# Kernel tuning notes

Hardware: AMD Instinct MI355X
Metric: run time of the kernel (lower is better)

Reference implementation:

```python
import jax, jax.numpy as jnp
import numpy as np

B, C, D, H, W = 4, 128, 24, 24, 24
P = 64


def _sparse_table(x):
    # Range-max sparse table along the last axis: level k holds max over
    # windows [i, i+2^k). Levels 0..3 (window sizes 1,2,4,8) suffice because
    # adaptive-pool region lengths are ceil(n/2) <= 12 for crop length n <= 24.
    tabs = [x]
    for k in range(1, 4):
        h = 1 << (k - 1)
        prev = tabs[-1]
        tabs.append(jnp.maximum(prev, jnp.roll(prev, -h, axis=-1)))
    return jnp.stack(tabs, 0)


def _klev(n):
    # floor(log2(n)) for n in [1, 12]
    return ((n >= 2).astype(jnp.int32) + (n >= 4).astype(jnp.int32)
            + (n >= 8).astype(jnp.int32))


def _bounds(s, e, size):
    # AdaptiveMaxPool (output size 2) region bounds along one axis.
    # crop is [s, min(e, size)); region o: [s + floor(o*n/2), s + ceil((o+1)*n/2))
    e = jnp.minimum(e, size)
    n = e - s  # crop length, always >= 2 here
    o = jnp.arange(2)
    start = s[..., None] + (o * n[..., None]) // 2
    end = s[..., None] + ((o + 1) * n[..., None] + 1) // 2
    return start, end


def _qmax(T, idx_prefix, sa, se):
    # Range max over [sa, se) along the last axis via two overlapping
    # power-of-two windows from the sparse table T ([L, ..., S]).
    k = _klev(se - sa)
    i2 = se - jnp.left_shift(1, k)
    lo = T[(k,) + idx_prefix + (Ellipsis, sa)]
    hi = T[(k,) + idx_prefix + (Ellipsis, i2)]
    return jnp.maximum(lo, hi)


def _crop_pool(fm, corners, scale):
    b, c, d, h, w = fm.shape
    p = corners.shape[1]
    # int(x/scale) with non-negative ints == floor division
    p1 = jnp.clip(corners[:, :, 0, :] // scale, 0, 21)   # [B,P,3]
    p2r = corners[:, :, 1, :] // scale
    p2 = jnp.where(p2r - p1 >= 2, p2r, p1 + 2)           # [B,P,3], p2 >= p1+2

    bi = jnp.arange(b)[:, None, None]                    # [B,1,1]
    pi = jnp.arange(p)[None, :, None]                    # [1,P,1]

    # reduce z (W axis): [B,C,D,H,W] -> [B,P,2(oz),C,D,H]
    sa, se = _bounds(p1[..., 2], p2[..., 2], w)
    r = _qmax(_sparse_table(fm), (bi,), sa, se)
    # reduce y (H axis): -> [B,P,2(oy),2(oz),C,D]
    sa, se = _bounds(p1[..., 1], p2[..., 1], h)
    r = _qmax(_sparse_table(r), (bi, pi), sa, se)
    # reduce x (D axis): -> [B,P,2(ox),2(oy),2(oz),C]
    sa, se = _bounds(p1[..., 0], p2[..., 0], d)
    r = _qmax(_sparse_table(r), (bi, pi), sa, se)
    # -> [B,P,C,2,2,2]
    return jnp.transpose(r, (0, 1, 5, 2, 3, 4))


def setup_inputs() -> dict:
    key = jax.random.key(0)
    k1, k2 = jax.random.split(key)
    fm = jax.random.normal(k1, (B, C, D, H, W), dtype=jnp.float32)
    corners = jax.random.randint(k2, (B, P, 2, 3), 0, 96, dtype=jnp.int32)
    return {"fm": fm, "corners": corners, "scale": 4}


def reference(fm, corners, scale):
    return _crop_pool(fm, corners, scale)
```

## Files before the change

### kernel.cpp

```cpp
#include <hip/hip_runtime.h>
#include <math.h>

#define Bc 4
#define Cc 128
#define Pc 64
#define PLANE 576
#define VOL   13824
#define NI    (-INFINITY)


struct Acc { float v00, v01, v10, v11; };

template<int RMODE>
__device__ __forceinline__ void upd(Acc& a, float t0, float t1) {
    if (RMODE != 1) { a.v00 = fmaxf(a.v00, t0); a.v01 = fmaxf(a.v01, t1); }
    if (RMODE != 0) { a.v10 = fmaxf(a.v10, t0); a.v11 = fmaxf(a.v11, t1); }
}

template<int RMODE>
__device__ __forceinline__ void plane_chunk(
    const float* __restrict__ p0, const float* __restrict__ p1,
    const float* __restrict__ p2, const float* __restrict__ p3,
    int fcl, const float4& B0, const float4& B1,
    Acc& a0, Acc& a1, Acc& a2, Acc& a3)
{
    float4 v0 = *(const float4*)(p0 + fcl);
    float4 v1 = *(const float4*)(p1 + fcl);
    float4 v2 = *(const float4*)(p2 + fcl);
    float4 v3 = *(const float4*)(p3 + fcl);
#define TREE(v, B) fmaxf(fmaxf((v).x + (B).x, (v).y + (B).y),              \
                         fmaxf((v).z + (B).z, (v).w + (B).w))
    upd<RMODE>(a0, TREE(v0, B0), TREE(v0, B1));
    upd<RMODE>(a1, TREE(v1, B0), TREE(v1, B1));
    upd<RMODE>(a2, TREE(v2, B0), TREE(v2, B1));
    upd<RMODE>(a3, TREE(v3, B0), TREE(v3, B1));
#undef TREE
}

__device__ __forceinline__ float oct_reduce(const float o[8], int lane) {
    const bool b0 = lane & 1, b1 = lane & 2, b2 = lane & 4;
    float m0 = fmaxf(b0 ? o[1] : o[0], __shfl_xor(b0 ? o[0] : o[1], 1));
    float m1 = fmaxf(b0 ? o[3] : o[2], __shfl_xor(b0 ? o[2] : o[3], 1));
    float m2 = fmaxf(b0 ? o[5] : o[4], __shfl_xor(b0 ? o[4] : o[5], 1));
    float m3 = fmaxf(b0 ? o[7] : o[6], __shfl_xor(b0 ? o[6] : o[7], 1));
    float n0 = fmaxf(b1 ? m1 : m0, __shfl_xor(b1 ? m0 : m1, 2));
    float n1 = fmaxf(b1 ? m3 : m2, __shfl_xor(b1 ? m2 : m3, 2));
    float v  = fmaxf(b2 ? n1 : n0, __shfl_xor(b2 ? n0 : n1, 4));
    v = fmaxf(v, __shfl_xor(v, 8));
    v = fmaxf(v, __shfl_xor(v, 16));
    v = fmaxf(v, __shfl_xor(v, 32));
    return v;
}

__global__ __launch_bounds__(256) void crop_pool_kernel(
    const float* __restrict__ fm, const int* __restrict__ corners,
    const int* __restrict__ scale_p, float* __restrict__ out)
{
    const int lane = threadIdx.x & 63;
    const int wid  = threadIdx.x >> 6;
    const int bp   = blockIdx.x >> 3;
    const int cg   = blockIdx.x & 7;
    const int slot = cg * 4 + wid;
    const int b    = bp >> 6;

    const float inv = 1.0f / (float)scale_p[0];

    int s[3], e[3], m0a[3], m1a[3];
#pragma unroll
    for (int k = 0; k < 3; ++k) {
        int c0 = corners[(bp * 2 + 0) * 3 + k];
        int c1 = corners[(bp * 2 + 1) * 3 + k];
        int p1v = (int)((float)c0 * inv);
        p1v = p1v > 21 ? 21 : p1v;
        int p2v = (int)((float)c1 * inv);
        if (p2v - p1v < 2) p2v = p1v + 2;
        int ee = p2v < 24 ? p2v : 24;
        int n  = ee - p1v;
        s[k]   = __builtin_amdgcn_readfirstlane(p1v);
        e[k]   = __builtin_amdgcn_readfirstlane(ee);
        m0a[k] = __builtin_amdgcn_readfirstlane(p1v + ((n + 1) >> 1));
        m1a[k] = __builtin_amdgcn_readfirstlane(p1v + (n >> 1));
    }

    const int sh  = s[1], eh = e[1], nh = eh - sh;
    const int m0h = m0a[1], m1h = m1a[1];
    const int sw  = s[2], ew = e[2], m0w = m0a[2], m1w = m1a[2];

    const int qb = sw & ~3;
    const int Q  = ((sw & 3) + (ew - sw) + 3) >> 2;
    const int R  = 64 / Q;

    const unsigned M = (65536u + (unsigned)Q - 1) / (unsigned)Q;
    const int r = (int)(((unsigned)lane * M) >> 16);
    const int q = lane - r * Q;
    const int wbase = qb + 4 * q;

    const bool c1p = nh > R;
    const bool c2p = nh > 2 * R;

    float4 B0, B1;
    {
        int wt;
        wt = wbase + 0;
        B0.x = (wt >= sw  && wt < m0w) ? 0.0f : NI;
        B1.x = (wt >= m1w && wt < ew ) ? 0.0f : NI;
        wt = wbase + 1;
        B0.y = (wt >= sw  && wt < m0w) ? 0.0f : NI;
        B1.y = (wt >= m1w && wt < ew ) ? 0.0f : NI;
        wt = wbase + 2;
        B0.z = (wt >= sw  && wt < m0w) ? 0.0f : NI;
        B1.z = (wt >= m1w && wt < ew ) ? 0.0f : NI;
        wt = wbase + 3;
        B0.w = (wt >= sw  && wt < m0w) ? 0.0f : NI;
        B1.w = (wt >= m1w && wt < ew ) ? 0.0f : NI;
    }

    int  fcl[3];
    bool h0m[3], h1m[3];
#pragma unroll
    for (int K = 0; K < 3; ++K) {
        const int h  = sh + K * R + r;
        const bool va = h < eh;
        const int  f  = h * 24 + wbase;
        fcl[K] = f < (PLANE - 4) ? f : (PLANE - 4);
        h0m[K] = va && (h <  m0h);
        h1m[K] = va && (h >= m1h);
    }

    Acc A[4][3];
#pragma unroll
    for (int i = 0; i < 4; ++i)
#pragma unroll
        for (int K = 0; K < 3; ++K) { A[i][K].v00=NI; A[i][K].v01=NI;
                                      A[i][K].v10=NI; A[i][K].v11=NI; }

    const float* pA = fm + ((size_t)(b * Cc + slot     )) * VOL + (size_t)s[0] * PLANE;
    const float* pB = fm + ((size_t)(b * Cc + slot + 32)) * VOL + (size_t)s[0] * PLANE;
    const float* pC = fm + ((size_t)(b * Cc + slot + 64)) * VOL + (size_t)s[0] * PLANE;
    const float* pD = fm + ((size_t)(b * Cc + slot + 96)) * VOL + (size_t)s[0] * PLANE;

#define STEP_AT(RM, OFF)                                                    \
    {                                                                       \
        plane_chunk<RM>(pA+(OFF), pB+(OFF), pC+(OFF), pD+(OFF), fcl[0],     \
                        B0, B1, A[0][0], A[1][0], A[2][0], A[3][0]);        \
        if (c1p) plane_chunk<RM>(pA+(OFF), pB+(OFF), pC+(OFF), pD+(OFF),    \
                        fcl[1], B0, B1, A[0][1], A[1][1], A[2][1], A[3][1]);\
        if (c2p) plane_chunk<RM>(pA+(OFF), pB+(OFF), pC+(OFF), pD+(OFF),    \
                        fcl[2], B0, B1, A[0][2], A[1][2], A[2][2], A[3][2]);\
    }
#define ADV(NP) { pA += (NP)*PLANE; pB += (NP)*PLANE; pC += (NP)*PLANE; pD += (NP)*PLANE; }

    int d = s[0];
    for (; d + 2 <= m1a[0]; d += 2) { STEP_AT(0, 0) STEP_AT(0, PLANE) ADV(2) }
    for (; d < m1a[0]; ++d)         { STEP_AT(0, 0) ADV(1) }
    for (; d < m0a[0]; ++d)         { STEP_AT(2, 0) ADV(1) }
    for (; d + 2 <= e[0]; d += 2)   { STEP_AT(1, 0) STEP_AT(1, PLANE) ADV(2) }
    for (; d < e[0]; ++d)           { STEP_AT(1, 0) ADV(1) }
#undef ADV
#undef STEP_AT

    float vch[4];
#pragma unroll
    for (int i = 0; i < 4; ++i) {
        float o[8];
#pragma unroll
        for (int j = 0; j < 8; ++j) o[j] = NI;
#pragma unroll
        for (int K = 0; K < 3; ++K) {
            if (K == 1 && !c1p) continue;
            if (K == 2 && !c2p) continue;
            o[0] = fmaxf(o[0], h0m[K] ? A[i][K].v00 : NI);
            o[1] = fmaxf(o[1], h0m[K] ? A[i][K].v01 : NI);
            o[2] = fmaxf(o[2], h1m[K] ? A[i][K].v00 : NI);
            o[3] = fmaxf(o[3], h1m[K] ? A[i][K].v01 : NI);
            o[4] = fmaxf(o[4], h0m[K] ? A[i][K].v10 : NI);
            o[5] = fmaxf(o[5], h0m[K] ? A[i][K].v11 : NI);
            o[6] = fmaxf(o[6], h1m[K] ? A[i][K].v10 : NI);
            o[7] = fmaxf(o[7], h1m[K] ? A[i][K].v11 : NI);
        }
        vch[i] = oct_reduce(o, lane);
    }

    if (lane < 32) {
        const float vv = (lane & 16) ? ((lane & 8) ? vch[3] : vch[2])
                                     : ((lane & 8) ? vch[1] : vch[0]);
        const int   cc = slot + 32 * (lane >> 3);
        out[((size_t)bp * Cc + cc) * 8 + (lane & 7)] = vv;
    }
}

extern "C" void kernel_launch(void* const* d_in, const int* in_sizes, int n_in,
                              void* d_out, int out_size, void* d_ws, size_t ws_size,
                              hipStream_t stream) {
    const float* fm      = (const float*)d_in[0];
    const int*   corners = (const int*)d_in[1];
    const int*   scale   = (const int*)d_in[2];
    float*       out     = (float*)d_out;

    dim3 grid(Bc * Pc * 8);
    dim3 block(256);
    crop_pool_kernel<<<grid, block, 0, stream>>>(fm, corners, scale, out);
}
```

Before: 23.34 us.

## Halve channels per wave, double grid, and fuse dual-channel reduction via half-wave shuffle

Each wave now handles 2 channels instead of 4, and the grid doubles to 4096 blocks, giving more waves to hide memory latency. The depth loop becomes a generic runtime loop with unroll 4 per segment, replacing the hand-unrolled two-plane steps. The final reduction merges the two channels' partial maxima with one xor-32 shuffle, then runs a single octant reduction instead of four separate ones. In exchange, per-block setup (corner decode, masks) is repeated twice as often and there is less load-level parallelism per thread.

```diff
diff --git a/kernel.cpp b/kernel.cpp
--- a/kernel.cpp
+++ b/kernel.cpp
@@ -17,39 +17,37 @@
     if (RMODE != 0) { a.v10 = fmaxf(a.v10, t0); a.v11 = fmaxf(a.v11, t1); }
 }
 
+#define TREE(v, B) fmaxf(fmaxf((v).x + (B).x, (v).y + (B).y),               \
+                         fmaxf((v).z + (B).z, (v).w + (B).w))
+
 template<int RMODE>
-__device__ __forceinline__ void plane_chunk(
-    const float* __restrict__ p0, const float* __restrict__ p1,
-    const float* __restrict__ p2, const float* __restrict__ p3,
-    int fcl, const float4& B0, const float4& B1,
-    Acc& a0, Acc& a1, Acc& a2, Acc& a3)
+__device__ __forceinline__ void run_seg(
+    const float* __restrict__& pA, const float* __restrict__& pB, int n,
+    bool c1p, bool c2p, const int fcl[3],
+    const float4 B0, const float4 B1, Acc* aA, Acc* aB)
 {
-    float4 v0 = *(const float4*)(p0 + fcl);
-    float4 v1 = *(const float4*)(p1 + fcl);
-    float4 v2 = *(const float4*)(p2 + fcl);
-    float4 v3 = *(const float4*)(p3 + fcl);
-#define TREE(v, B) fmaxf(fmaxf((v).x + (B).x, (v).y + (B).y),              \
-                         fmaxf((v).z + (B).z, (v).w + (B).w))
-    upd<RMODE>(a0, TREE(v0, B0), TREE(v0, B1));
-    upd<RMODE>(a1, TREE(v1, B0), TREE(v1, B1));
-    upd<RMODE>(a2, TREE(v2, B0), TREE(v2, B1));
-    upd<RMODE>(a3, TREE(v3, B0), TREE(v3, B1));
-#undef TREE
-}
-
-__device__ __forceinline__ float oct_reduce(const float o[8], int lane) {
-    const bool b0 = lane & 1, b1 = lane & 2, b2 = lane & 4;
-    float m0 = fmaxf(b0 ? o[1] : o[0], __shfl_xor(b0 ? o[0] : o[1], 1));
-    float m1 = fmaxf(b0 ? o[3] : o[2], __shfl_xor(b0 ? o[2] : o[3], 1));
-    float m2 = fmaxf(b0 ? o[5] : o[4], __shfl_xor(b0 ? o[4] : o[5], 1));
-    float m3 = fmaxf(b0 ? o[7] : o[6], __shfl_xor(b0 ? o[6] : o[7], 1));
-    float n0 = fmaxf(b1 ? m1 : m0, __shfl_xor(b1 ? m0 : m1, 2));
-    float n1 = fmaxf(b1 ? m3 : m2, __shfl_xor(b1 ? m2 : m3, 2));
-    float v  = fmaxf(b2 ? n1 : n0, __shfl_xor(b2 ? n0 : n1, 4));
-    v = fmaxf(v, __shfl_xor(v, 8));
-    v = fmaxf(v, __shfl_xor(v, 16));
-    v = fmaxf(v, __shfl_xor(v, 32));
-    return v;
+#pragma unroll 4
+    for (int i = 0; i < n; ++i) {
+        {
+            float4 vA = *(const float4*)(pA + fcl[0]);
+            float4 vB = *(const float4*)(pB + fcl[0]);
+            upd<RMODE>(aA[0], TREE(vA, B0), TREE(vA, B1));
+            upd<RMODE>(aB[0], TREE(vB, B0), TREE(vB, B1));
+        }
+        if (c1p) {
+            float4 vA = *(const float4*)(pA + fcl[1]);
+            float4 vB = *(const float4*)(pB + fcl[1]);
+            upd<RMODE>(aA[1], TREE(vA, B0), TREE(vA, B1));
+            upd<RMODE>(aB[1], TREE(vB, B0), TREE(vB, B1));
+        }
+        if (c2p) {
+            float4 vA = *(const float4*)(pA + fcl[2]);
+            float4 vB = *(const float4*)(pB + fcl[2]);
+            upd<RMODE>(aA[2], TREE(vA, B0), TREE(vA, B1));
+            upd<RMODE>(aB[2], TREE(vB, B0), TREE(vB, B1));
+        }
+        pA += PLANE; pB += PLANE;
+    }
 }
 
 __global__ __launch_bounds__(256) void crop_pool_kernel(
@@ -58,9 +56,11 @@
 {
     const int lane = threadIdx.x & 63;
     const int wid  = threadIdx.x >> 6;
-    const int bp   = blockIdx.x >> 3;
-    const int cg   = blockIdx.x & 7;
+    const int bp   = blockIdx.x >> 4;
+    const int cg   = blockIdx.x & 15;
     const int slot = cg * 4 + wid;
+    const int cA   = slot;
+    const int cB   = slot + 64;
     const int b    = bp >> 6;
 
     const float inv = 1.0f / (float)scale_p[0];
@@ -119,7 +119,7 @@
     bool h0m[3], h1m[3];
 #pragma unroll
     for (int K = 0; K < 3; ++K) {
-        const int h  = sh + K * R + r;
+        const int  h  = sh + K * R + r;
         const bool va = h < eh;
         const int  f  = h * 24 + wbase;
         fcl[K] = f < (PLANE - 4) ? f : (PLANE - 4);
@@ -127,65 +127,69 @@
         h1m[K] = va && (h >= m1h);
     }
 
-    Acc A[4][3];
-#pragma unroll
-    for (int i = 0; i < 4; ++i)
-#pragma unroll
-        for (int K = 0; K < 3; ++K) { A[i][K].v00=NI; A[i][K].v01=NI;
-                                      A[i][K].v10=NI; A[i][K].v11=NI; }
-
-    const float* pA = fm + ((size_t)(b * Cc + slot     )) * VOL + (size_t)s[0] * PLANE;
-    const float* pB = fm + ((size_t)(b * Cc + slot + 32)) * VOL + (size_t)s[0] * PLANE;
-    const float* pC = fm + ((size_t)(b * Cc + slot + 64)) * VOL + (size_t)s[0] * PLANE;
-    const float* pD = fm + ((size_t)(b * Cc + slot + 96)) * VOL + (size_t)s[0] * PLANE;
-
-#define STEP_AT(RM, OFF)                                                    \
-    {                                                                       \
-        plane_chunk<RM>(pA+(OFF), pB+(OFF), pC+(OFF), pD+(OFF), fcl[0],     \
-                        B0, B1, A[0][0], A[1][0], A[2][0], A[3][0]);        \
-        if (c1p) plane_chunk<RM>(pA+(OFF), pB+(OFF), pC+(OFF), pD+(OFF),    \
-                        fcl[1], B0, B1, A[0][1], A[1][1], A[2][1], A[3][1]);\
-        if (c2p) plane_chunk<RM>(pA+(OFF), pB+(OFF), pC+(OFF), pD+(OFF),    \
-                        fcl[2], B0, B1, A[0][2], A[1][2], A[2][2], A[3][2]);\
-    }
-#define ADV(NP) { pA += (NP)*PLANE; pB += (NP)*PLANE; pC += (NP)*PLANE; pD += (NP)*PLANE; }
-
-    int d = s[0];
-    for (; d + 2 <= m1a[0]; d += 2) { STEP_AT(0, 0) STEP_AT(0, PLANE) ADV(2) }
-    for (; d < m1a[0]; ++d)         { STEP_AT(0, 0) ADV(1) }
-    for (; d < m0a[0]; ++d)         { STEP_AT(2, 0) ADV(1) }
-    for (; d + 2 <= e[0]; d += 2)   { STEP_AT(1, 0) STEP_AT(1, PLANE) ADV(2) }
-    for (; d < e[0]; ++d)           { STEP_AT(1, 0) ADV(1) }
-#undef ADV
-#undef STEP_AT
-
-    float vch[4];
-#pragma unroll
-    for (int i = 0; i < 4; ++i) {
-        float o[8];
-#pragma unroll
-        for (int j = 0; j < 8; ++j) o[j] = NI;
-#pragma unroll
-        for (int K = 0; K < 3; ++K) {
-            if (K == 1 && !c1p) continue;
-            if (K == 2 && !c2p) continue;
-            o[0] = fmaxf(o[0], h0m[K] ? A[i][K].v00 : NI);
-            o[1] = fmaxf(o[1], h0m[K] ? A[i][K].v01 : NI);
-            o[2] = fmaxf(o[2], h1m[K] ? A[i][K].v00 : NI);
-            o[3] = fmaxf(o[3], h1m[K] ? A[i][K].v01 : NI);
-            o[4] = fmaxf(o[4], h0m[K] ? A[i][K].v10 : NI);
-            o[5] = fmaxf(o[5], h0m[K] ? A[i][K].v11 : NI);
-            o[6] = fmaxf(o[6], h1m[K] ? A[i][K].v10 : NI);
-            o[7] = fmaxf(o[7], h1m[K] ? A[i][K].v11 : NI);
-        }
-        vch[i] = oct_reduce(o, lane);
-    }
-
-    if (lane < 32) {
-        const float vv = (lane & 16) ? ((lane & 8) ? vch[3] : vch[2])
-                                     : ((lane & 8) ? vch[1] : vch[0]);
-        const int   cc = slot + 32 * (lane >> 3);
-        out[((size_t)bp * Cc + cc) * 8 + (lane & 7)] = vv;
+    Acc aA[3], aB[3];
+#pragma unroll
+    for (int K = 0; K < 3; ++K) {
+        aA[K].v00=NI; aA[K].v01=NI; aA[K].v10=NI; aA[K].v11=NI;
+        aB[K].v00=NI; aB[K].v01=NI; aB[K].v10=NI; aB[K].v11=NI;
+    }
+
+    const float* __restrict__ pA =
+        fm + ((size_t)(b * Cc + cA)) * VOL + (size_t)s[0] * PLANE;
+    const float* __restrict__ pB =
+        fm + ((size_t)(b * Cc + cB)) * VOL + (size_t)s[0] * PLANE;
+
+    run_seg<0>(pA, pB, m1a[0] - s[0],   c1p, c2p, fcl, B0, B1, aA, aB);
+    run_seg<2>(pA, pB, m0a[0] - m1a[0], c1p, c2p, fcl, B0, B1, aA, aB);
+    run_seg<1>(pA, pB, e[0]  - m0a[0],  c1p, c2p, fcl, B0, B1, aA, aB);
+
+    float oA[8], oB[8];
+#pragma unroll
+    for (int j = 0; j < 8; ++j) { oA[j] = NI; oB[j] = NI; }
+#pragma unroll
+    for (int K = 0; K < 3; ++K) {
+        if (K == 1 && !c1p) continue;
+        if (K == 2 && !c2p) continue;
+        oA[0] = fmaxf(oA[0], h0m[K] ? aA[K].v00 : NI);
+        oA[1] = fmaxf(oA[1], h0m[K] ? aA[K].v01 : NI);
+        oA[2] = fmaxf(oA[2], h1m[K] ? aA[K].v00 : NI);
+        oA[3] = fmaxf(oA[3], h1m[K] ? aA[K].v01 : NI);
+        oA[4] = fmaxf(oA[4], h0m[K] ? aA[K].v10 : NI);
+        oA[5] = fmaxf(oA[5], h0m[K] ? aA[K].v11 : NI);
+        oA[6] = fmaxf(oA[6], h1m[K] ? aA[K].v10 : NI);
+        oA[7] = fmaxf(oA[7], h1m[K] ? aA[K].v11 : NI);
+        oB[0] = fmaxf(oB[0], h0m[K] ? aB[K].v00 : NI);
+        oB[1] = fmaxf(oB[1], h0m[K] ? aB[K].v01 : NI);
+        oB[2] = fmaxf(oB[2], h1m[K] ? aB[K].v00 : NI);
+        oB[3] = fmaxf(oB[3], h1m[K] ? aB[K].v01 : NI);
+        oB[4] = fmaxf(oB[4], h0m[K] ? aB[K].v10 : NI);
+        oB[5] = fmaxf(oB[5], h0m[K] ? aB[K].v11 : NI);
+        oB[6] = fmaxf(oB[6], h1m[K] ? aB[K].v10 : NI);
+        oB[7] = fmaxf(oB[7], h1m[K] ? aB[K].v11 : NI);
+    }
+
+    const bool lo = lane < 32;
+    float x[8];
+#pragma unroll
+    for (int j = 0; j < 8; ++j) {
+        float keep = lo ? oA[j] : oB[j];
+        float send = lo ? oB[j] : oA[j];
+        x[j] = fmaxf(keep, __shfl_xor(send, 32));
+    }
+    const bool b0 = lane & 1, b1 = lane & 2, b2 = lane & 4;
+    float m0_ = fmaxf(b0 ? x[1] : x[0], __shfl_xor(b0 ? x[0] : x[1], 1));
+    float m1_ = fmaxf(b0 ? x[3] : x[2], __shfl_xor(b0 ? x[2] : x[3], 1));
+    float m2_ = fmaxf(b0 ? x[5] : x[4], __shfl_xor(b0 ? x[4] : x[5], 1));
+    float m3_ = fmaxf(b0 ? x[7] : x[6], __shfl_xor(b0 ? x[6] : x[7], 1));
+    float n0_ = fmaxf(b1 ? m1_ : m0_, __shfl_xor(b1 ? m0_ : m1_, 2));
+    float n1_ = fmaxf(b1 ? m3_ : m2_, __shfl_xor(b1 ? m2_ : m3_, 2));
+    float v   = fmaxf(b2 ? n1_ : n0_, __shfl_xor(b2 ? n0_ : n1_, 4));
+    v = fmaxf(v, __shfl_xor(v, 8));
+    v = fmaxf(v, __shfl_xor(v, 16));
+
+    if ((lane & 31) < 8) {
+        const int cc = lo ? cA : cB;
+        out[((size_t)bp * Cc + cc) * 8 + (lane & 7)] = v;
     }
 }
 
@@ -197,7 +201,7 @@
     const int*   scale   = (const int*)d_in[2];
     float*       out     = (float*)d_out;
 
-    dim3 grid(Bc * Pc * 8);
+    dim3 grid(Bc * Pc * 16);
     dim3 block(256);
     crop_pool_kernel<<<grid, block, 0, stream>>>(fm, corners, scale, out);
 }
```

Result: no change. 23.64 us (+1.3%).
